# Optimization experiments

Measured on AMD Instinct MI355X. Metric: run time of the kernel, lower is better.

Reference implementation:

```python
import jax, jax.numpy as jnp
import numpy as np
from jax import lax

COS_BASIS_NO = 24
SCALE = 6.0
SHIFT = 1.0


def make_kern_basis(T_no):
    # [24, T_no] raised-cosine log-time basis, matching the torch loop exactly
    i = jnp.arange(COS_BASIS_NO, dtype=jnp.float32)
    phi = (jnp.pi / 2.0) * i                                  # [24]
    x = jnp.arange(T_no, dtype=jnp.float32)
    raw = SCALE * jnp.log(x + SHIFT + 1e-7)                   # [T_no]
    basis = 0.5 * jnp.cos(raw[None, :] - phi[:, None]) + 0.5  # [24, T_no]
    inside = (raw[None, :] >= phi[:, None] - jnp.pi) & (raw[None, :] <= phi[:, None] + jnp.pi)
    return jnp.where(inside, basis, 0.0)


def causal_grouped_conv(x, kern, sub_no, T_no):
    # x: [B, sub_no, T], kern: [sub_no*hid, T_no] (already flipped like torch)
    # left-pad T_no-1 zeros == the torch zero-padded buffer; cross-correlation
    rhs = kern[:, None, :]  # OIH with I=1 per group
    return lax.conv_general_dilated(
        x, rhs, window_strides=(1,), padding=[(T_no - 1, 0)],
        feature_group_count=sub_no,
        dimension_numbers=("NCH", "OIH", "NCH"))


def setup_inputs() -> dict:
    key = jax.random.key(0)
    ks = jax.random.split(key, 10)
    B, T_data = 8, 5000
    sub_no, E_no, I_no, T_no, hid_no = 20, 2000, 200, 400, 16
    inp = {
        "S_e": jax.random.uniform(ks[0], (B, T_data, E_no), dtype=jnp.float32),
        "S_i": jax.random.uniform(ks[1], (B, T_data, I_no), dtype=jnp.float32),
        "E_scale": jnp.zeros((E_no,), jnp.float32),
        "I_scale": jnp.zeros((I_no,), jnp.float32),
        "W_e_layer1": jax.random.normal(ks[2], (sub_no * hid_no, COS_BASIS_NO), jnp.float32) * 0.01,
        "W_i_layer1": jax.random.normal(ks[3], (sub_no * hid_no, COS_BASIS_NO), jnp.float32) * 0.01,
        "W_layer2": jnp.full((sub_no, hid_no), -1.0, jnp.float32),
        "b_layer1": jnp.zeros((sub_no * hid_no,), jnp.float32),
        "C_syn_e_raw": jax.random.normal(ks[4], (sub_no, E_no), jnp.float32) * 0.01,
        "C_syn_i_raw": jax.random.normal(ks[5], (sub_no, I_no), jnp.float32) * 0.01,
        "V_o": jnp.zeros((1,), jnp.float32),
        "temp": jnp.asarray(1.0, jnp.float32),
        "T_no": T_no,
        "test": 1,
    }
    return inp


def reference(S_e, S_i, E_scale, I_scale, W_e_layer1, W_i_layer1, W_layer2,
              b_layer1, C_syn_e_raw, C_syn_i_raw, V_o, temp, T_no, test):
    sub_no = C_syn_e_raw.shape[0]
    hid_no = W_layer2.shape[1]
    B, T_data, _ = S_e.shape

    if test:
        C_syn_e = jax.nn.softmax(C_syn_e_raw / temp, axis=0)
        C_syn_i = jax.nn.softmax(C_syn_i_raw / temp, axis=0)
    else:
        eps = 1e-8
        ku, kv = jax.random.split(jax.random.key(42))
        u_e = jax.random.uniform(ku, C_syn_e_raw.shape, dtype=C_syn_e_raw.dtype)
        u_i = jax.random.uniform(kv, C_syn_i_raw.shape, dtype=C_syn_i_raw.dtype)
        g_e = -jnp.log(-jnp.log(u_e + eps) + eps)
        g_i = -jnp.log(-jnp.log(u_i + eps) + eps)
        C_syn_e = jax.nn.softmax((C_syn_e_raw + g_e) / temp, axis=0)
        C_syn_i = jax.nn.softmax((C_syn_i_raw + g_i) / temp, axis=0)

    # scale synapses and project onto subunits: [B,T,E] x [E,sub] -> [B,T,sub]
    syn_e = jnp.einsum("bte,se->bts", S_e * jnp.exp(E_scale)[None, None, :], C_syn_e)
    syn_i = jnp.einsum("bti,si->bts", S_i * jnp.exp(I_scale)[None, None, :], C_syn_i)

    kern_basis = make_kern_basis(T_no)                        # [24, T_no]
    ke = jnp.flip(W_e_layer1 @ kern_basis, axis=1)            # [sub*hid, T_no]
    ki = jnp.flip(W_i_layer1 @ kern_basis, axis=1)

    xe = jnp.transpose(syn_e, (0, 2, 1))                      # [B, sub, T]
    xi = jnp.transpose(syn_i, (0, 2, 1))
    conv_e = causal_grouped_conv(xe, ke, sub_no, T_no)        # [B, sub*hid, T]
    conv_i = causal_grouped_conv(xi, ki, sub_no, T_no)
    layer1 = jnp.tanh(conv_e + conv_i + b_layer1[None, :, None])

    # grouped 1x1 conv == per-subunit weighted reduction over hid
    h = layer1.reshape(B, sub_no, hid_no, T_data)
    sub_out = jnp.einsum("bshT,sh->bTs", h, jnp.exp(W_layer2))  # [B, T, sub]
    final = jnp.sum(sub_out, axis=-1) + V_o                    # [B, T]
    return final, sub_out, C_syn_e, C_syn_i
```

## Files before the change

kernel.cpp:

```cpp
#include <hip/hip_runtime.h>
#include <math.h>

#define PI_F 3.14159265358979323846f
#define BSTRIDE 404

__global__ __launch_bounds__(256) void prep_kernel(
    const float* __restrict__ Ce_raw, const float* __restrict__ Ci_raw,
    const float* __restrict__ Escale, const float* __restrict__ Iscale,
    const float* __restrict__ temp,
    float* __restrict__ CsT_e, float* __restrict__ CsT_i,
    float* __restrict__ basis,
    float* __restrict__ outCe, float* __restrict__ outCi)
{
    int id = blockIdx.x * 256 + threadIdx.x;
    if (id < 2000) {
        int e = id;
        float t = temp[0];
        float v[20];
        float m = -1e30f;
        #pragma unroll
        for (int s = 0; s < 20; ++s) { v[s] = Ce_raw[s * 2000 + e] / t; m = fmaxf(m, v[s]); }
        float sum = 0.f;
        #pragma unroll
        for (int s = 0; s < 20; ++s) { v[s] = expf(v[s] - m); sum += v[s]; }
        float inv = 1.f / sum;
        float sc = expf(Escale[e]);
        #pragma unroll
        for (int s = 0; s < 20; ++s) {
            float p = v[s] * inv;
            outCe[s * 2000 + e] = p;
            CsT_e[e * 20 + s] = p * sc;
        }
    } else if (id < 2200) {
        int e = id - 2000;
        float t = temp[0];
        float v[20];
        float m = -1e30f;
        #pragma unroll
        for (int s = 0; s < 20; ++s) { v[s] = Ci_raw[s * 200 + e] / t; m = fmaxf(m, v[s]); }
        float sum = 0.f;
        #pragma unroll
        for (int s = 0; s < 20; ++s) { v[s] = expf(v[s] - m); sum += v[s]; }
        float inv = 1.f / sum;
        float sc = expf(Iscale[e]);
        #pragma unroll
        for (int s = 0; s < 20; ++s) {
            float p = v[s] * inv;
            outCi[s * 200 + e] = p;
            CsT_i[e * 20 + s] = p * sc;
        }
    } else if (id < 2200 + 24 * BSTRIDE) {
        int idx = id - 2200;
        int j = idx / BSTRIDE, d = idx - j * BSTRIDE;
        float val = 0.f;
        if (d < 400) {
            float raw = 6.0f * logf((float)d + 1.0f + 1e-7f);
            float ph = (PI_F * 0.5f) * (float)j;
            if (raw >= ph - PI_F && raw <= ph + PI_F) val = 0.5f * cosf(raw - ph) + 0.5f;
        }
        basis[idx] = val;
    } else if (id < 11896 + 48) {
        int row = 2000 + (id - 11896);
        #pragma unroll
        for (int s = 0; s < 20; ++s) CsT_e[row * 20 + s] = 0.f;
    } else if (id < 11944 + 56) {
        int row = 200 + (id - 11944);
        #pragma unroll
        for (int s = 0; s < 20; ++s) CsT_i[row * 20 + s] = 0.f;
    }
}

template <int NCHUNK>
__global__ __launch_bounds__(256) void syn_kernel(
    const float* __restrict__ S, const float* __restrict__ CsT,
    float* __restrict__ syn, int Eno)
{
    __shared__ float4 tile[64 * 33];
    float* red = reinterpret_cast<float*>(tile);
    const int tid = threadIdx.x;
    const int lane = tid & 63;
    const int w = __builtin_amdgcn_readfirstlane(tid >> 6);
    const int r0 = blockIdx.x * 64;

    float acc[20];
    #pragma unroll
    for (int s = 0; s < 20; ++s) acc[s] = 0.f;

    for (int ch = 0; ch < NCHUNK; ++ch) {
        const int ebase = ch * 128;
        #pragma unroll
        for (int i = 0; i < 8; ++i) {
            int f = tid + i * 256;
            int row = f >> 5, col4 = f & 31;
            int e0 = ebase + col4 * 4;
            float4 v = make_float4(0.f, 0.f, 0.f, 0.f);
            if (e0 + 4 <= Eno)
                v = *reinterpret_cast<const float4*>(S + (size_t)(r0 + row) * Eno + e0);
            tile[row * 33 + col4] = v;
        }
        __syncthreads();

        const float4* crow = reinterpret_cast<const float4*>(CsT + (size_t)(ebase + w * 32) * 20);
        #pragma unroll
        for (int c4 = 0; c4 < 8; ++c4) {
            float4 v = tile[lane * 33 + w * 8 + c4];
            const float4* ct = crow + c4 * 20;
            float vv[4] = {v.x, v.y, v.z, v.w};
            #pragma unroll
            for (int q = 0; q < 4; ++q) {
                float sv = vv[q];
                #pragma unroll
                for (int c5 = 0; c5 < 5; ++c5) {
                    float4 cc = ct[q * 5 + c5];
                    acc[c5 * 4 + 0] = fmaf(sv, cc.x, acc[c5 * 4 + 0]);
                    acc[c5 * 4 + 1] = fmaf(sv, cc.y, acc[c5 * 4 + 1]);
                    acc[c5 * 4 + 2] = fmaf(sv, cc.z, acc[c5 * 4 + 2]);
                    acc[c5 * 4 + 3] = fmaf(sv, cc.w, acc[c5 * 4 + 3]);
                }
            }
        }
        __syncthreads();
    }

    #pragma unroll
    for (int s = 0; s < 20; ++s) red[(lane * 4 + w) * 20 + s] = acc[s];
    __syncthreads();

    #pragma unroll
    for (int i = 0; i < 5; ++i) {
        int p = tid + i * 256;
        int row = p & 63, s = p >> 6;
        float a = red[(row * 4 + 0) * 20 + s] + red[(row * 4 + 1) * 20 + s]
                + red[(row * 4 + 2) * 20 + s] + red[(row * 4 + 3) * 20 + s];
        int r = r0 + row;
        int b = r / 5000, t = r - b * 5000;
        syn[((size_t)b * 20 + s) * 5000 + t] = a;
    }
}

__device__ const int CJ_LO[24] = {0,0,0,0,0,0,0,0,0,4,4,8,12,16,20,28,36,48,64,84,108,140,184,240};
__device__ const int CJ_NB[24] = {1,1,1,1,2,2,3,3,4,4,5,6,7,9,12,15,19,25,31,41,53,65,54,40};

__global__ __launch_bounds__(256) void conv_kernel(
    const float* __restrict__ syn_e, const float* __restrict__ syn_i,
    const float* __restrict__ basis,
    const float* __restrict__ W_e, const float* __restrict__ W_i,
    const float* __restrict__ b1, const float* __restrict__ W2,
    float* __restrict__ sub_out)
{
    __shared__ float4 win4[804];
    float2* win2 = reinterpret_cast<float2*>(win4);
    const int tid = threadIdx.x;
    const int tile = blockIdx.x, s = blockIdx.y, bz = blockIdx.z;
    const int t0 = tile * 1024;

    const float* se = syn_e + ((size_t)bz * 20 + s) * 5000;
    const float* si = syn_i + ((size_t)bz * 20 + s) * 5000;
    for (int l = tid; l < 1428; l += 256) {
        int t = t0 - 404 + l;
        float ve = 0.f, vi = 0.f;
        if ((unsigned)t < 5000u) { ve = se[t]; vi = si[t]; }
        int g = l >> 1;
        win2[2 * (g + (g >> 3)) + (l & 1)] = make_float2(ve, vi);
    }
    __syncthreads();

    float z[16][4];
    #pragma unroll
    for (int h = 0; h < 16; ++h) {
        float bv = b1[s * 16 + h];
        #pragma unroll
        for (int k = 0; k < 4; ++k) z[h][k] = bv;
    }

    const int base = 4 * tid + 400;

    for (int j = 0; j < 24; ++j) {
        const float4* bj4 = reinterpret_cast<const float4*>(basis + j * BSTRIDE);
        const int lo = CJ_LO[j];
        const int nb = CJ_NB[j];
        float be0 = 0.f, be1 = 0.f, be2 = 0.f, be3 = 0.f;
        float bi0 = 0.f, bi1 = 0.f, bi2 = 0.f, bi3 = 0.f;

        int g = (base - lo) >> 1;
        float4 V0 = win4[g + (g >> 3)];
        float4 V1 = win4[(g + 1) + ((g + 1) >> 3)];
        float4 V2 = win4[(g + 2) + ((g + 2) >> 3)];
        float4 V3 = win4[(g + 3) + ((g + 3) >> 3)];
        float4 C = bj4[lo >> 2];

        for (int bb = 0; bb < nb; ++bb) {
            float4 Cn = bj4[(lo >> 2) + bb + 1];
            be0 = fmaf(C.x, V2.x, be0); bi0 = fmaf(C.x, V2.y, bi0);
            be1 = fmaf(C.x, V2.z, be1); bi1 = fmaf(C.x, V2.w, bi1);
            be2 = fmaf(C.x, V3.x, be2); bi2 = fmaf(C.x, V3.y, bi2);
            be3 = fmaf(C.x, V3.z, be3); bi3 = fmaf(C.x, V3.w, bi3);
            be0 = fmaf(C.y, V1.z, be0); bi0 = fmaf(C.y, V1.w, bi0);
            be1 = fmaf(C.y, V2.x, be1); bi1 = fmaf(C.y, V2.y, bi1);
            be2 = fmaf(C.y, V2.z, be2); bi2 = fmaf(C.y, V2.w, bi2);
            be3 = fmaf(C.y, V3.x, be3); bi3 = fmaf(C.y, V3.y, bi3);
            be0 = fmaf(C.z, V1.x, be0); bi0 = fmaf(C.z, V1.y, bi0);
            be1 = fmaf(C.z, V1.z, be1); bi1 = fmaf(C.z, V1.w, bi1);
            be2 = fmaf(C.z, V2.x, be2); bi2 = fmaf(C.z, V2.y, bi2);
            be3 = fmaf(C.z, V2.z, be3); bi3 = fmaf(C.z, V2.w, bi3);
            be0 = fmaf(C.w, V0.z, be0); bi0 = fmaf(C.w, V0.w, bi0);
            be1 = fmaf(C.w, V1.x, be1); bi1 = fmaf(C.w, V1.y, bi1);
            be2 = fmaf(C.w, V1.z, be2); bi2 = fmaf(C.w, V1.w, bi2);
            be3 = fmaf(C.w, V2.x, be3); bi3 = fmaf(C.w, V2.y, bi3);
            V3 = V1; V2 = V0;
            g -= 2;
            V0 = win4[g + (g >> 3)];
            V1 = win4[(g + 1) + ((g + 1) >> 3)];
            C = Cn;
        }

        #pragma unroll
        for (int h = 0; h < 16; ++h) {
            float we = W_e[(s * 16 + h) * 24 + j];
            float wi = W_i[(s * 16 + h) * 24 + j];
            z[h][0] = fmaf(we, be0, fmaf(wi, bi0, z[h][0]));
            z[h][1] = fmaf(we, be1, fmaf(wi, bi1, z[h][1]));
            z[h][2] = fmaf(we, be2, fmaf(wi, bi2, z[h][2]));
            z[h][3] = fmaf(we, be3, fmaf(wi, bi3, z[h][3]));
        }
    }

    float w2v[16];
    #pragma unroll
    for (int h = 0; h < 16; ++h) w2v[h] = __expf(W2[s * 16 + h]);

    #pragma unroll
    for (int k = 0; k < 4; ++k) {
        int t = t0 + 4 * tid + k;
        if (t < 5000) {
            float acc = 0.f;
            #pragma unroll
            for (int h = 0; h < 16; ++h) {
                float e2 = __expf(2.0f * z[h][k]);
                float th = 1.0f - 2.0f / (e2 + 1.0f);
                acc = fmaf(w2v[h], th, acc);
            }
            sub_out[((size_t)bz * 5000 + t) * 20 + s] = acc;
        }
    }
}

__global__ __launch_bounds__(256) void final_kernel(
    const float* __restrict__ sub_out, const float* __restrict__ V_o,
    float* __restrict__ fin)
{
    int r = blockIdx.x * 256 + threadIdx.x;
    if (r < 40000) {
        const float* p = sub_out + (size_t)r * 20;
        float a = V_o[0];
        #pragma unroll
        for (int s = 0; s < 20; ++s) a += p[s];
        fin[r] = a;
    }
}

extern "C" void kernel_launch(void* const* d_in, const int* in_sizes, int n_in,
                              void* d_out, int out_size, void* d_ws, size_t ws_size,
                              hipStream_t stream)
{
    const float* S_e     = (const float*)d_in[0];
    const float* S_i     = (const float*)d_in[1];
    const float* E_scale = (const float*)d_in[2];
    const float* I_scale = (const float*)d_in[3];
    const float* W_e     = (const float*)d_in[4];
    const float* W_i     = (const float*)d_in[5];
    const float* W2      = (const float*)d_in[6];
    const float* b1      = (const float*)d_in[7];
    const float* Ce_raw  = (const float*)d_in[8];
    const float* Ci_raw  = (const float*)d_in[9];
    const float* V_o     = (const float*)d_in[10];
    const float* temp    = (const float*)d_in[11];

    float* out     = (float*)d_out;
    float* fin     = out;
    float* sub_out = out + 40000;
    float* outCe   = out + 840000;
    float* outCi   = out + 880000;

    float* ws    = (float*)d_ws;
    float* CsT_e = ws;
    float* CsT_i = ws + 40960;
    float* basis = ws + 46080;
    float* syn_e = ws + 55776;
    float* syn_i = ws + 855776;

    prep_kernel<<<47, 256, 0, stream>>>(Ce_raw, Ci_raw, E_scale, I_scale, temp,
                                        CsT_e, CsT_i, basis, outCe, outCi);
    syn_kernel<16><<<625, 256, 0, stream>>>(S_e, CsT_e, syn_e, 2000);
    syn_kernel<2><<<625, 256, 0, stream>>>(S_i, CsT_i, syn_i, 200);
    conv_kernel<<<dim3(5, 20, 8), 256, 0, stream>>>(syn_e, syn_i, basis,
                                                    W_e, W_i, b1, W2, sub_out);
    final_kernel<<<157, 256, 0, stream>>>(sub_out, V_o, fin);
}
```

Before: 336.4 us.

## Halve conv tile size, swizzle LDS window layout, unroll basis loop by two

The conv kernel now uses 128-thread blocks over 512-step tiles, doubling the grid to 1600 blocks so more blocks can run at once. The shared-memory window moves from padded indexing to a swizzled layout (phys4) that splits each float4 pair across two banks groups. The inner basis loop is unrolled by two, swapping register roles instead of copying them, and reads scalar basis coefficients instead of prefetched float4s. Smaller tiles mean a larger relative halo to load (404 samples per 512 outputs), and the scalar coefficient loads add load instructions.

```diff
diff --git a/kernel.cpp b/kernel.cpp
--- a/kernel.cpp
+++ b/kernel.cpp
@@ -141,27 +141,31 @@
 __device__ const int CJ_LO[24] = {0,0,0,0,0,0,0,0,0,4,4,8,12,16,20,28,36,48,64,84,108,140,184,240};
 __device__ const int CJ_NB[24] = {1,1,1,1,2,2,3,3,4,4,5,6,7,9,12,15,19,25,31,41,53,65,54,40};
 
-__global__ __launch_bounds__(256) void conv_kernel(
+__device__ __forceinline__ int phys4(int g) {
+    return (g & ~15) | ((g >> 1) & 7) | ((g & 1) << 3);
+}
+
+__global__ __launch_bounds__(128) void conv_kernel(
     const float* __restrict__ syn_e, const float* __restrict__ syn_i,
     const float* __restrict__ basis,
     const float* __restrict__ W_e, const float* __restrict__ W_i,
     const float* __restrict__ b1, const float* __restrict__ W2,
     float* __restrict__ sub_out)
 {
-    __shared__ float4 win4[804];
+    __shared__ float4 win4[464];
     float2* win2 = reinterpret_cast<float2*>(win4);
     const int tid = threadIdx.x;
     const int tile = blockIdx.x, s = blockIdx.y, bz = blockIdx.z;
-    const int t0 = tile * 1024;
+    const int t0 = tile * 512;
 
     const float* se = syn_e + ((size_t)bz * 20 + s) * 5000;
     const float* si = syn_i + ((size_t)bz * 20 + s) * 5000;
-    for (int l = tid; l < 1428; l += 256) {
+    for (int l = tid; l < 920; l += 128) {
         int t = t0 - 404 + l;
         float ve = 0.f, vi = 0.f;
         if ((unsigned)t < 5000u) { ve = se[t]; vi = si[t]; }
         int g = l >> 1;
-        win2[2 * (g + (g >> 3)) + (l & 1)] = make_float2(ve, vi);
+        win2[2 * phys4(g) + (l & 1)] = make_float2(ve, vi);
     }
     __syncthreads();
 
@@ -176,43 +180,53 @@
     const int base = 4 * tid + 400;
 
     for (int j = 0; j < 24; ++j) {
-        const float4* bj4 = reinterpret_cast<const float4*>(basis + j * BSTRIDE);
+        const float* bj = basis + j * BSTRIDE;
         const int lo = CJ_LO[j];
         const int nb = CJ_NB[j];
         float be0 = 0.f, be1 = 0.f, be2 = 0.f, be3 = 0.f;
         float bi0 = 0.f, bi1 = 0.f, bi2 = 0.f, bi3 = 0.f;
 
+        auto body = [&](const float4& V0, const float4& V1,
+                        const float4& V2, const float4& V3, int dd0) {
+            float c0 = bj[dd0], c1 = bj[dd0 + 1], c2 = bj[dd0 + 2], c3 = bj[dd0 + 3];
+            be0 = fmaf(c0, V2.x, be0); bi0 = fmaf(c0, V2.y, bi0);
+            be1 = fmaf(c0, V2.z, be1); bi1 = fmaf(c0, V2.w, bi1);
+            be2 = fmaf(c0, V3.x, be2); bi2 = fmaf(c0, V3.y, bi2);
+            be3 = fmaf(c0, V3.z, be3); bi3 = fmaf(c0, V3.w, bi3);
+            be0 = fmaf(c1, V1.z, be0); bi0 = fmaf(c1, V1.w, bi0);
+            be1 = fmaf(c1, V2.x, be1); bi1 = fmaf(c1, V2.y, bi1);
+            be2 = fmaf(c1, V2.z, be2); bi2 = fmaf(c1, V2.w, bi2);
+            be3 = fmaf(c1, V3.x, be3); bi3 = fmaf(c1, V3.y, bi3);
+            be0 = fmaf(c2, V1.x, be0); bi0 = fmaf(c2, V1.y, bi0);
+            be1 = fmaf(c2, V1.z, be1); bi1 = fmaf(c2, V1.w, bi1);
+            be2 = fmaf(c2, V2.x, be2); bi2 = fmaf(c2, V2.y, bi2);
+            be3 = fmaf(c2, V2.z, be3); bi3 = fmaf(c2, V2.w, bi3);
+            be0 = fmaf(c3, V0.z, be0); bi0 = fmaf(c3, V0.w, bi0);
+            be1 = fmaf(c3, V1.x, be1); bi1 = fmaf(c3, V1.y, bi1);
+            be2 = fmaf(c3, V1.z, be2); bi2 = fmaf(c3, V1.w, bi2);
+            be3 = fmaf(c3, V2.x, be3); bi3 = fmaf(c3, V2.y, bi3);
+        };
+
         int g = (base - lo) >> 1;
-        float4 V0 = win4[g + (g >> 3)];
-        float4 V1 = win4[(g + 1) + ((g + 1) >> 3)];
-        float4 V2 = win4[(g + 2) + ((g + 2) >> 3)];
-        float4 V3 = win4[(g + 3) + ((g + 3) >> 3)];
-        float4 C = bj4[lo >> 2];
-
-        for (int bb = 0; bb < nb; ++bb) {
-            float4 Cn = bj4[(lo >> 2) + bb + 1];
-            be0 = fmaf(C.x, V2.x, be0); bi0 = fmaf(C.x, V2.y, bi0);
-            be1 = fmaf(C.x, V2.z, be1); bi1 = fmaf(C.x, V2.w, bi1);
-            be2 = fmaf(C.x, V3.x, be2); bi2 = fmaf(C.x, V3.y, bi2);
-            be3 = fmaf(C.x, V3.z, be3); bi3 = fmaf(C.x, V3.w, bi3);
-            be0 = fmaf(C.y, V1.z, be0); bi0 = fmaf(C.y, V1.w, bi0);
-            be1 = fmaf(C.y, V2.x, be1); bi1 = fmaf(C.y, V2.y, bi1);
-            be2 = fmaf(C.y, V2.z, be2); bi2 = fmaf(C.y, V2.w, bi2);
-            be3 = fmaf(C.y, V3.x, be3); bi3 = fmaf(C.y, V3.y, bi3);
-            be0 = fmaf(C.z, V1.x, be0); bi0 = fmaf(C.z, V1.y, bi0);
-            be1 = fmaf(C.z, V1.z, be1); bi1 = fmaf(C.z, V1.w, bi1);
-            be2 = fmaf(C.z, V2.x, be2); bi2 = fmaf(C.z, V2.y, bi2);
-            be3 = fmaf(C.z, V2.z, be3); bi3 = fmaf(C.z, V2.w, bi3);
-            be0 = fmaf(C.w, V0.z, be0); bi0 = fmaf(C.w, V0.w, bi0);
-            be1 = fmaf(C.w, V1.x, be1); bi1 = fmaf(C.w, V1.y, bi1);
-            be2 = fmaf(C.w, V1.z, be2); bi2 = fmaf(C.w, V1.w, bi2);
-            be3 = fmaf(C.w, V2.x, be3); bi3 = fmaf(C.w, V2.y, bi3);
-            V3 = V1; V2 = V0;
-            g -= 2;
-            V0 = win4[g + (g >> 3)];
-            V1 = win4[(g + 1) + ((g + 1) >> 3)];
-            C = Cn;
-        }
+        int pa = phys4(g);
+        int pb = phys4(g + 2);
+        float4 a0 = win4[pa], a1 = win4[pa + 8];
+        float4 b0 = win4[pb], b1v = win4[pb + 8];
+
+        int d0 = lo;
+        int bb = 0;
+        for (; bb + 2 <= nb; bb += 2) {
+            body(a0, a1, b0, b1v, d0);
+            int pn = phys4(g - 2);
+            b0 = win4[pn]; b1v = win4[pn + 8];
+            body(b0, b1v, a0, a1, d0 + 4);
+            pn = phys4(g - 4);
+            a0 = win4[pn]; a1 = win4[pn + 8];
+            g -= 4;
+            d0 += 8;
+        }
+        if (bb < nb)
+            body(a0, a1, b0, b1v, d0);
 
         #pragma unroll
         for (int h = 0; h < 16; ++h) {
@@ -293,7 +307,7 @@
                                         CsT_e, CsT_i, basis, outCe, outCi);
     syn_kernel<16><<<625, 256, 0, stream>>>(S_e, CsT_e, syn_e, 2000);
     syn_kernel<2><<<625, 256, 0, stream>>>(S_i, CsT_i, syn_i, 200);
-    conv_kernel<<<dim3(5, 20, 8), 256, 0, stream>>>(syn_e, syn_i, basis,
-                                                    W_e, W_i, b1, W2, sub_out);
+    conv_kernel<<<dim3(10, 20, 8), 128, 0, stream>>>(syn_e, syn_i, basis,
+                                                     W_e, W_i, b1, W2, sub_out);
     final_kernel<<<157, 256, 0, stream>>>(sub_out, V_o, fin);
 }
```

Measured after the change: 289.1 us. 14.0% less time.
